# Kernel tuning notes

Hardware: AMD Instinct MI355X
Metric: run time of the kernel (lower is better)

## Reference

```python
import jax, jax.numpy as jnp
import numpy as np

EPS = 1e-5
NUM_HEADS = 8


def _ln(x, w, b):
    m = x.mean(-1, keepdims=True)
    v = jnp.mean(jnp.square(x - m), -1, keepdims=True)
    return (x - m) * jax.lax.rsqrt(v + EPS) * w + b


def _bn(x, w, b, mean, var):  # x: [N, C, T], eval-mode BatchNorm1d
    return (x - mean[None, :, None]) * jax.lax.rsqrt(var[None, :, None] + EPS) * w[None, :, None] + b[None, :, None]


def setup_inputs() -> dict:
    key = jax.random.key(0)
    ks = jax.random.split(key, 32)
    B, T, E, C = 8, 64, 128, 256
    H = 2 * C       # temporal conv hidden
    M = 4 * C       # mlp hidden
    s = 0.02
    f32 = jnp.float32
    inp = {
        'x': jax.random.normal(ks[0], (B, T, E, C), f32),
        'adj_mask': jax.random.randint(ks[1], (E, E), 0, 2, jnp.int32),
        'n1_w': 1.0 + s * jax.random.normal(ks[2], (C,), f32),
        'n1_b': s * jax.random.normal(ks[3], (C,), f32),
        'q_w': s * jax.random.normal(ks[4], (C, C), f32),
        'k_w': s * jax.random.normal(ks[5], (C, C), f32),
        'v_w': s * jax.random.normal(ks[6], (C, C), f32),
        'proj_w': s * jax.random.normal(ks[7], (C, C), f32),
        'proj_b': s * jax.random.normal(ks[8], (C,), f32),
        'on_w': 1.0 + s * jax.random.normal(ks[9], (C,), f32),
        'on_b': s * jax.random.normal(ks[10], (C,), f32),
        'gamma_s': jnp.asarray([0.5], f32),
        'conv1_w': s * jax.random.normal(ks[11], (H, C, 3), f32),
        'bn1_w': 1.0 + s * jax.random.normal(ks[12], (H,), f32),
        'bn1_b': s * jax.random.normal(ks[13], (H,), f32),
        'bn1_m': s * jax.random.normal(ks[14], (H,), f32),
        'bn1_v': jax.random.uniform(ks[15], (H,), f32, 0.5, 1.5),
        'conv2_w': s * jax.random.normal(ks[16], (C, H, 1), f32),
        'bn2_w': 1.0 + s * jax.random.normal(ks[17], (C,), f32),
        'bn2_b': s * jax.random.normal(ks[18], (C,), f32),
        'bn2_m': s * jax.random.normal(ks[19], (C,), f32),
        'bn2_v': jax.random.uniform(ks[20], (C,), f32, 0.5, 1.5),
        'tn_w': 1.0 + s * jax.random.normal(ks[21], (C,), f32),
        'tn_b': s * jax.random.normal(ks[22], (C,), f32),
        'gamma_t': jnp.asarray([0.5], f32),
        'n3_w': 1.0 + s * jax.random.normal(ks[23], (C,), f32),
        'n3_b': s * jax.random.normal(ks[24], (C,), f32),
        'fc1_w': s * jax.random.normal(ks[25], (C, M), f32),
        'fc1_b': s * jax.random.normal(ks[26], (M,), f32),
        'fc2_w': s * jax.random.normal(ks[27], (M, C), f32),
        'fc2_b': s * jax.random.normal(ks[28], (C,), f32),
    }
    return inp


def reference(x, adj_mask, n1_w, n1_b, q_w, k_w, v_w, proj_w, proj_b, on_w, on_b,
              gamma_s, conv1_w, bn1_w, bn1_b, bn1_m, bn1_v, conv2_w, bn2_w, bn2_b,
              bn2_m, bn2_v, tn_w, tn_b, gamma_t, n3_w, n3_b, fc1_w, fc1_b, fc2_w, fc2_b):
    B, T, E, C = x.shape
    Hh = NUM_HEADS
    D = C // Hh
    mask = adj_mask.astype(x.dtype)

    # ---- spatial geometric-cosine attention (per frame) ----
    xs = _ln(x, n1_w, n1_b)                                   # norm1
    q = (xs @ q_w).reshape(B, T, E, Hh, D)
    k = (xs @ k_w).reshape(B, T, E, Hh, D)
    v = (xs @ v_w).reshape(B, T, E, Hh, D)
    attn = jnp.einsum('btehd,btfhd->bthef', q, k)             # [B,T,H,E,E]
    attn = (attn * mask[None, None, None] + 1.0) * 0.5        # affine mask, no softmax
    o = jnp.einsum('bthef,btfhd->btehd', attn, v).reshape(B, T, E, C)
    o = _ln(o @ proj_w + proj_b, on_w, on_b)                  # proj + output_norm
    x = x + (xs + gamma_s * o)                                # inner + outer residual

    # ---- temporal convolution (norm2 is Identity) ----
    xt = _ln(x, tn_w, tn_b)
    xc = xt.transpose(0, 2, 3, 1).reshape(B * E, C, T)        # 'b t e c -> (b e) c t'
    dn = ('NCH', 'OIH', 'NCH')
    y = jax.lax.conv_general_dilated(xc, conv1_w, (1,), [(1, 1)], dimension_numbers=dn)
    y = jax.nn.gelu(_bn(y, bn1_w, bn1_b, bn1_m, bn1_v), approximate=False)
    y = jax.lax.conv_general_dilated(y, conv2_w, (1,), [(0, 0)], dimension_numbers=dn)
    y = _bn(y, bn2_w, bn2_b, bn2_m, bn2_v)
    y = y.reshape(B, E, C, T).transpose(0, 3, 1, 2)           # '(b e) c t -> b t e c'
    x = x + (x + gamma_t * y)                                 # temporal inner + outer residual

    # ---- MLP ----
    xm = _ln(x, n3_w, n3_b)
    h = jax.nn.gelu(xm @ fc1_w + fc1_b, approximate=False)
    x = x + (h @ fc2_w + fc2_b)
    return x
```

## Files before the change

kernel.cpp:

```cpp
#include <hip/hip_runtime.h>
#include <cstdint>

constexpr int Bn = 8, Tn = 64, En = 128, Cn = 256;
constexpr int Hn = 512, Mn = 1024, NHd = 8, Dn = 32;
constexpr int NTOK = Bn * Tn * En;
constexpr size_t SZ = (size_t)NTOK * Cn;
#define EPSF 1e-5f

typedef __attribute__((ext_vector_type(8))) short short8;
typedef __attribute__((ext_vector_type(4))) float f32x4;

__device__ __forceinline__ float bf2f(unsigned short u) {
  union { unsigned int i; float f; } c; c.i = ((unsigned int)u) << 16; return c.f;
}
__device__ __forceinline__ unsigned short f2bf(float f) {
  union { float f; unsigned int i; } c; c.f = f;
  unsigned int u = c.i;
  return (unsigned short)((u + 0x7fffu + ((u >> 16) & 1u)) >> 16);
}
__device__ __forceinline__ float gelu_f(float v) {
  return 0.5f * v * (1.0f + erff(v * 0.70710678118654752440f));
}

__device__ __forceinline__ void gload16(const unsigned short* g, unsigned short* l) {
  __builtin_amdgcn_global_load_lds(
      (const __attribute__((address_space(1))) unsigned int*)g,
      (__attribute__((address_space(3))) unsigned int*)l, 16, 0, 0);
}

template <int EPI, bool C1A>
__global__ __launch_bounds__(256) void mfma_gemm(
    const unsigned short* __restrict__ A,
    const unsigned short* __restrict__ Bt,
    const float* __restrict__ scale,
    const float* __restrict__ bias,
    const float* __restrict__ resf,
    const float* __restrict__ gscal,
    void* __restrict__ outv,
    int K, int N) {
  __shared__ unsigned short As[128 * 32];
  __shared__ unsigned short Bs[128 * 32];
  int tid = threadIdx.x;
  int lane = tid & 63, wave = tid >> 6;
  int mtile = blockIdx.y, ntile = blockIdx.x;
  int rowBase = mtile * 128;
  int colBase = ntile * 128;
  int lda = C1A ? 256 : K;
  int r0 = lane >> 2;
  int c0 = (lane & 3) * 8;
  f32x4 acc[4][4];
#pragma unroll
  for (int i = 0; i < 4; ++i)
#pragma unroll
    for (int j = 0; j < 4; ++j) acc[i][j] = (f32x4)(0.0f);
  int mbase = (wave >> 1) * 64;
  int nbase = (wave & 1) * 64;
  int arow = lane & 15;
  int akk = (lane >> 4) * 8;

  for (int k0 = 0; k0 < K; k0 += 32) {
    size_t arowb; int kin;
    if (C1A) {
      int bb = mtile >> 6, tt = mtile & 63;
      int slab = k0 >> 8;
      arowb = (size_t)((bb * 66 + tt + slab) * 128);
      kin = k0 & 255;
    } else {
      arowb = (size_t)rowBase;
      kin = k0;
    }
#pragma unroll
    for (int i = 0; i < 2; ++i) {
      int q = i * 4 + wave;
      const unsigned short* gp = A + (arowb + q * 16 + r0) * (size_t)lda + kin + c0;
      gload16(gp, &As[q * 512]);
      const unsigned short* gq = Bt + ((size_t)colBase + q * 16 + r0) * (size_t)K + k0 + c0;
      gload16(gq, &Bs[q * 512]);
    }
    __syncthreads();
    short8 af[4], bf[4];
#pragma unroll
    for (int i = 0; i < 4; ++i)
      af[i] = *(const short8*)&As[(mbase + i * 16 + arow) * 32 + akk];
#pragma unroll
    for (int j = 0; j < 4; ++j)
      bf[j] = *(const short8*)&Bs[(nbase + j * 16 + arow) * 32 + akk];
#pragma unroll
    for (int i = 0; i < 4; ++i)
#pragma unroll
      for (int j = 0; j < 4; ++j)
        acc[i][j] = __builtin_amdgcn_mfma_f32_16x16x32_bf16(af[i], bf[j], acc[i][j], 0, 0, 0);
    __syncthreads();
  }

  int crow0 = (lane >> 4) * 4;
  int ccol = lane & 15;
  float gt = (EPI == 3) ? gscal[0] : 0.f;
#pragma unroll
  for (int i = 0; i < 4; ++i) {
#pragma unroll
    for (int j = 0; j < 4; ++j) {
      int col = colBase + nbase + j * 16 + ccol;
      float sc = 1.f, bi = 0.f;
      if (EPI >= 1 && bias) bi = bias[col];
      if ((EPI == 2 || EPI == 3) && scale) sc = scale[col];
#pragma unroll
      for (int r = 0; r < 4; ++r) {
        size_t row = (size_t)rowBase + mbase + i * 16 + crow0 + r;
        size_t idx = row * (size_t)N + col;
        float v = acc[i][j][r];
        if (EPI == 0)      ((unsigned short*)outv)[idx] = f2bf(v);
        else if (EPI == 1) ((unsigned short*)outv)[idx] = f2bf(v + bi);
        else if (EPI == 2) ((unsigned short*)outv)[idx] = f2bf(gelu_f(v * sc + bi));
        else if (EPI == 3) ((float*)outv)[idx] = 2.0f * resf[idx] + gt * (v * sc + bi);
        else if (EPI == 4) ((float*)outv)[idx] = resf[idx] + v + bi;
        else if (EPI == 5) ((float*)outv)[idx] = v + bi;
      }
    }
  }
}

template <bool PAD>
__global__ __launch_bounds__(256) void ln256_bf(const float* __restrict__ src,
                                                const float* __restrict__ w,
                                                const float* __restrict__ b,
                                                unsigned short* __restrict__ dst) {
  int lane = threadIdx.x & 63;
  int tok = blockIdx.x * 4 + (threadIdx.x >> 6);
  const float4* row = (const float4*)(src + (size_t)tok * Cn);
  float4 v = row[lane];
  float s  = v.x + v.y + v.z + v.w;
  float s2 = v.x*v.x + v.y*v.y + v.z*v.z + v.w*v.w;
#pragma unroll
  for (int off = 32; off >= 1; off >>= 1) {
    s  += __shfl_xor(s, off, 64);
    s2 += __shfl_xor(s2, off, 64);
  }
  float mean = s * (1.0f / Cn);
  float var = fmaxf(s2 * (1.0f / Cn) - mean * mean, 0.0f);
  float r = rsqrtf(var + EPSF);
  float4 wv = ((const float4*)w)[lane];
  float4 bv = ((const float4*)b)[lane];
  size_t dtok = tok;
  if (PAD) {
    int bb = tok >> 13, tt = (tok >> 7) & 63, e = tok & 127;
    dtok = ((size_t)(bb * 66 + tt + 1)) * 128 + e;
  }
  ushort4 o;
  o.x = f2bf((v.x - mean) * r * wv.x + bv.x);
  o.y = f2bf((v.y - mean) * r * wv.y + bv.y);
  o.z = f2bf((v.z - mean) * r * wv.z + bv.z);
  o.w = f2bf((v.w - mean) * r * wv.w + bv.w);
  *(ushort4*)(dst + dtok * Cn + lane * 4) = o;
}

__global__ __launch_bounds__(256) void attn_mfma(const unsigned short* __restrict__ qkv,
                                                 const float* __restrict__ maskh,
                                                 unsigned short* __restrict__ o) {
  __shared__ unsigned short Qs[128 * 32];
  __shared__ unsigned short Ks[128 * 32];
  __shared__ unsigned short Vt[32 * 136];
  __shared__ unsigned short Ps[128 * 136];
  int tid = threadIdx.x, lane = tid & 63, wave = tid >> 6;
  int h = blockIdx.x & 7, bt = blockIdx.x >> 3;
  size_t gbase = (size_t)bt * 128 * 768 + h * 32;
#pragma unroll
  for (int i = 0; i < 2; ++i) {
    int q = wave * 2 + i;
    int row = q * 16 + (lane >> 2);
    int seg = (lane & 3) * 8;
    gload16(qkv + gbase + (size_t)row * 768 + seg, &Qs[q * 512]);
    gload16(qkv + gbase + 256 + (size_t)row * 768 + seg, &Ks[q * 512]);
  }
  {
    int e = tid >> 1, dh = (tid & 1) * 16;
    const unsigned short* gv = qkv + gbase + 512 + (size_t)e * 768 + dh;
    short8 v0 = *(const short8*)gv;
    short8 v1 = *(const short8*)(gv + 8);
#pragma unroll
    for (int j = 0; j < 8; ++j) {
      Vt[(dh + j) * 136 + e]     = (unsigned short)v0[j];
      Vt[(dh + 8 + j) * 136 + e] = (unsigned short)v1[j];
    }
  }
  __syncthreads();
  int arow = lane & 15, akk = (lane >> 4) * 8;
  int crow0 = (lane >> 4) * 4, ccol = lane & 15;
  short8 af0 = *(const short8*)&Qs[(wave * 32 + arow) * 32 + akk];
  short8 af1 = *(const short8*)&Qs[(wave * 32 + 16 + arow) * 32 + akk];
#pragma unroll
  for (int j = 0; j < 8; ++j) {
    short8 bfr = *(const short8*)&Ks[(j * 16 + arow) * 32 + akk];
    f32x4 s0 = __builtin_amdgcn_mfma_f32_16x16x32_bf16(af0, bfr, (f32x4)(0.0f), 0, 0, 0);
    f32x4 s1 = __builtin_amdgcn_mfma_f32_16x16x32_bf16(af1, bfr, (f32x4)(0.0f), 0, 0, 0);
    int f = j * 16 + ccol;
#pragma unroll
    for (int r = 0; r < 4; ++r) {
      int e0 = wave * 32 + crow0 + r;
      int e1 = e0 + 16;
      Ps[e0 * 136 + f] = f2bf(maskh[e0 * 128 + f] * s0[r] + 0.5f);
      Ps[e1 * 136 + f] = f2bf(maskh[e1 * 128 + f] * s1[r] + 0.5f);
    }
  }
  f32x4 acc[2][2];
#pragma unroll
  for (int i = 0; i < 2; ++i)
#pragma unroll
    for (int j = 0; j < 2; ++j) acc[i][j] = (f32x4)(0.0f);
#pragma unroll
  for (int k0 = 0; k0 < 128; k0 += 32) {
    short8 a0 = *(const short8*)&Ps[(wave * 32 + arow) * 136 + k0 + akk];
    short8 a1 = *(const short8*)&Ps[(wave * 32 + 16 + arow) * 136 + k0 + akk];
    short8 b0 = *(const short8*)&Vt[arow * 136 + k0 + akk];
    short8 b1 = *(const short8*)&Vt[(16 + arow) * 136 + k0 + akk];
    acc[0][0] = __builtin_amdgcn_mfma_f32_16x16x32_bf16(a0, b0, acc[0][0], 0, 0, 0);
    acc[0][1] = __builtin_amdgcn_mfma_f32_16x16x32_bf16(a0, b1, acc[0][1], 0, 0, 0);
    acc[1][0] = __builtin_amdgcn_mfma_f32_16x16x32_bf16(a1, b0, acc[1][0], 0, 0, 0);
    acc[1][1] = __builtin_amdgcn_mfma_f32_16x16x32_bf16(a1, b1, acc[1][1], 0, 0, 0);
  }
  unsigned short* ob = o + (size_t)bt * 128 * 256 + h * 32;
#pragma unroll
  for (int i = 0; i < 2; ++i)
#pragma unroll
    for (int j = 0; j < 2; ++j)
#pragma unroll
      for (int r = 0; r < 4; ++r) {
        int e = wave * 32 + i * 16 + crow0 + r;
        ob[(size_t)e * 256 + j * 16 + ccol] = f2bf(acc[i][j][r]);
      }
}

__global__ __launch_bounds__(256) void resid1_kernel(const float* __restrict__ x,
                                                     const unsigned short* __restrict__ xs,
                                                     const unsigned short* __restrict__ p2,
                                                     const float* __restrict__ gs,
                                                     float* __restrict__ x1) {
  size_t i = ((size_t)blockIdx.x * 256 + threadIdx.x) * 4;
  float g = gs[0];
  float4 xv = *(const float4*)(x + i);
  ushort4 s4 = *(const ushort4*)(xs + i);
  ushort4 p4 = *(const ushort4*)(p2 + i);
  float4 r;
  r.x = xv.x + bf2f(s4.x) + g * bf2f(p4.x);
  r.y = xv.y + bf2f(s4.y) + g * bf2f(p4.y);
  r.z = xv.z + bf2f(s4.z) + g * bf2f(p4.z);
  r.w = xv.w + bf2f(s4.w) + g * bf2f(p4.w);
  *(float4*)(x1 + i) = r;
}

__global__ __launch_bounds__(256) void transcast(const float* __restrict__ src,
                                                 unsigned short* __restrict__ dst,
                                                 int N, int K) {
  int idx = blockIdx.x * 256 + threadIdx.x;
  int n = idx / K, k = idx - n * K;
  dst[idx] = f2bf(src[(size_t)k * N + n]);
}
__global__ __launch_bounds__(256) void castbf(const float* __restrict__ s,
                                              unsigned short* __restrict__ d) {
  int i = blockIdx.x * 256 + threadIdx.x;
  d[i] = f2bf(s[i]);
}
__global__ __launch_bounds__(256) void pack_conv1(const float* __restrict__ w1,
                                                  unsigned short* __restrict__ dst) {
  int idx = blockIdx.x * 256 + threadIdx.x;
  int hh = idx / 768, kk = idx - hh * 768;
  int slab = kk >> 8, c = kk & 255;
  dst[idx] = f2bf(w1[(size_t)hh * 768 + c * 3 + slab]);
}
__global__ __launch_bounds__(256) void bnfold(const float* __restrict__ w,
                                              const float* __restrict__ bvec,
                                              const float* __restrict__ m,
                                              const float* __restrict__ v,
                                              float* __restrict__ s,
                                              float* __restrict__ o, int n) {
  int i = blockIdx.x * 256 + threadIdx.x;
  if (i < n) {
    float sc = w[i] * rsqrtf(v[i] + EPSF);
    s[i] = sc;
    o[i] = bvec[i] - m[i] * sc;
  }
}
__global__ __launch_bounds__(256) void mask_prep(const int* __restrict__ adj,
                                                 float* __restrict__ maskh) {
  int i = blockIdx.x * 256 + threadIdx.x;
  maskh[i] = 0.5f * (float)adj[i];
}
__global__ __launch_bounds__(256) void zero_pad(unsigned short* __restrict__ xt) {
  int idx = blockIdx.x * 256 + threadIdx.x;
  int bb = idx >> 16;
  int rem = idx & 65535;
  int which = rem >> 15;
  int off = rem & 32767;
  size_t base = ((size_t)(bb * 66 + which * 65)) * 128 * 256;
  xt[base + off] = 0;
}

extern "C" void kernel_launch(void* const* d_in, const int* in_sizes, int n_in,
                              void* d_out, int out_size, void* d_ws, size_t ws_size,
                              hipStream_t stream) {
  (void)in_sizes; (void)n_in; (void)out_size; (void)ws_size;
  const float* x       = (const float*)d_in[0];
  const int*   adj     = (const int*)  d_in[1];
  const float* n1_w    = (const float*)d_in[2];
  const float* n1_b    = (const float*)d_in[3];
  const float* q_w     = (const float*)d_in[4];
  const float* k_w     = (const float*)d_in[5];
  const float* v_w     = (const float*)d_in[6];
  const float* proj_w  = (const float*)d_in[7];
  const float* proj_b  = (const float*)d_in[8];
  const float* on_w    = (const float*)d_in[9];
  const float* on_b    = (const float*)d_in[10];
  const float* gamma_s = (const float*)d_in[11];
  const float* conv1_w = (const float*)d_in[12];
  const float* bn1_w   = (const float*)d_in[13];
  const float* bn1_b   = (const float*)d_in[14];
  const float* bn1_m   = (const float*)d_in[15];
  const float* bn1_v   = (const float*)d_in[16];
  const float* conv2_w = (const float*)d_in[17];
  const float* bn2_w   = (const float*)d_in[18];
  const float* bn2_b   = (const float*)d_in[19];
  const float* bn2_m   = (const float*)d_in[20];
  const float* bn2_v   = (const float*)d_in[21];
  const float* tn_w    = (const float*)d_in[22];
  const float* tn_b    = (const float*)d_in[23];
  const float* gamma_t = (const float*)d_in[24];
  const float* n3_w    = (const float*)d_in[25];
  const float* n3_b    = (const float*)d_in[26];
  const float* fc1_w   = (const float*)d_in[27];
  const float* fc1_b   = (const float*)d_in[28];
  const float* fc2_w   = (const float*)d_in[29];
  const float* fc2_b   = (const float*)d_in[30];
  float* O = (float*)d_out;

  const size_t MB = 1024 * 1024;
  char* wsb = (char*)d_ws;
  unsigned short* qkvb = (unsigned short*)(wsb + 0);
  float*          pjo  = (float*)(wsb + 0);
  float*          x1b  = (float*)(wsb + 0);
  unsigned short* xmb  = (unsigned short*)(wsb + 0);
  unsigned short* hb   = (unsigned short*)(wsb + 32 * MB);
  unsigned short* xtp  = (unsigned short*)(wsb + 64 * MB);
  unsigned short* xsb  = (unsigned short*)(wsb + 96 * MB);
  unsigned short* oat  = (unsigned short*)(wsb + 128 * MB);
  unsigned short* p2b  = (unsigned short*)(wsb + 128 * MB);
  unsigned short* y1b  = (unsigned short*)(wsb + 100 * MB);
  char* wp = wsb + 164 * MB;
  unsigned short* Wqkv = (unsigned short*)wp;  wp += 768 * 256 * 2;
  unsigned short* PjT  = (unsigned short*)wp;  wp += 256 * 256 * 2;
  unsigned short* W1t  = (unsigned short*)wp;  wp += 512 * 768 * 2;
  unsigned short* W2t  = (unsigned short*)wp;  wp += 256 * 512 * 2;
  unsigned short* F1t  = (unsigned short*)wp;  wp += 1024 * 256 * 2;
  unsigned short* F2t  = (unsigned short*)wp;  wp += 256 * 1024 * 2;
  float* s1 = (float*)wp; wp += 512 * 4;
  float* o1 = (float*)wp; wp += 512 * 4;
  float* s2 = (float*)wp; wp += 256 * 4;
  float* o2 = (float*)wp; wp += 256 * 4;
  float* maskh = (float*)wp; wp += 16384 * 4;

  transcast<<<768 * 256 / 256, 256, 0, stream>>>(q_w, Wqkv, 256, 256);
  transcast<<<768 * 256 / 256, 256, 0, stream>>>(k_w, Wqkv + 256 * 256, 256, 256);
  transcast<<<768 * 256 / 256, 256, 0, stream>>>(v_w, Wqkv + 512 * 256, 256, 256);
  transcast<<<256 * 256 / 256, 256, 0, stream>>>(proj_w, PjT, 256, 256);
  pack_conv1<<<512 * 768 / 256, 256, 0, stream>>>(conv1_w, W1t);
  castbf<<<256 * 512 / 256, 256, 0, stream>>>(conv2_w, W2t);
  transcast<<<1024 * 256 / 256, 256, 0, stream>>>(fc1_w, F1t, 1024, 256);
  transcast<<<256 * 1024 / 256, 256, 0, stream>>>(fc2_w, F2t, 256, 1024);
  bnfold<<<2, 256, 0, stream>>>(bn1_w, bn1_b, bn1_m, bn1_v, s1, o1, 512);
  bnfold<<<1, 256, 0, stream>>>(bn2_w, bn2_b, bn2_m, bn2_v, s2, o2, 256);
  mask_prep<<<64, 256, 0, stream>>>(adj, maskh);
  zero_pad<<<524288 / 256, 256, 0, stream>>>(xtp);

  ln256_bf<false><<<NTOK / 4, 256, 0, stream>>>(x, n1_w, n1_b, xsb);
  mfma_gemm<0, false><<<dim3(6, 512), 256, 0, stream>>>(xsb, Wqkv, nullptr, nullptr, nullptr, nullptr, qkvb, 256, 768);
  attn_mfma<<<Bn * Tn * NHd, 256, 0, stream>>>(qkvb, maskh, oat);
  mfma_gemm<5, false><<<dim3(2, 512), 256, 0, stream>>>(oat, PjT, nullptr, proj_b, nullptr, nullptr, pjo, 256, 256);
  ln256_bf<false><<<NTOK / 4, 256, 0, stream>>>(pjo, on_w, on_b, p2b);
  resid1_kernel<<<(int)(SZ / (4 * 256)), 256, 0, stream>>>(x, xsb, p2b, gamma_s, x1b);

  ln256_bf<true><<<NTOK / 4, 256, 0, stream>>>(x1b, tn_w, tn_b, xtp);
  mfma_gemm<2, true><<<dim3(4, 512), 256, 0, stream>>>(xtp, W1t, s1, o1, nullptr, nullptr, y1b, 768, 512);
  mfma_gemm<3, false><<<dim3(2, 512), 256, 0, stream>>>(y1b, W2t, s2, o2, x1b, gamma_t, O, 512, 256);

  ln256_bf<false><<<NTOK / 4, 256, 0, stream>>>(O, n3_w, n3_b, xmb);
  mfma_gemm<2, false><<<dim3(8, 512), 256, 0, stream>>>(xmb, F1t, nullptr, fc1_b, nullptr, nullptr, hb, 256, 1024);
  mfma_gemm<4, false><<<dim3(2, 512), 256, 0, stream>>>(hb, F2t, nullptr, fc2_b, O, nullptr, O, 1024, 256);
}
```

Before: 742.3 us.

## Double-buffer LDS tiles in MFMA GEMM and swizzle workgroups across XCDs

The GEMM main loop now uses two LDS buffers so the global-to-LDS loads for the next K-slice are issued before the MFMAs on the current slice run, with explicit vmcnt waits and barriers replacing the two __syncthreads per iteration. Block indices are also remapped so that consecutive tiles land on the same XCD chiplet, which should improve L2 reuse. The cost is doubled LDS use, which may lower occupancy. The swizzle assumes the grid size is divisible by 8, and the loop assumes an even number of K-steps of at least two.

```diff
diff --git a/kernel.cpp b/kernel.cpp
--- a/kernel.cpp
+++ b/kernel.cpp
@@ -27,6 +27,8 @@
       (const __attribute__((address_space(1))) unsigned int*)g,
       (__attribute__((address_space(3))) unsigned int*)l, 16, 0, 0);
 }
+
+#define MEMFENCE() asm volatile("" ::: "memory")
 
 template <int EPI, bool C1A>
 __global__ __launch_bounds__(256) void mfma_gemm(
@@ -38,11 +40,18 @@
     const float* __restrict__ gscal,
     void* __restrict__ outv,
     int K, int N) {
-  __shared__ unsigned short As[128 * 32];
-  __shared__ unsigned short Bs[128 * 32];
+  __shared__ unsigned short As[2][128 * 32];
+  __shared__ unsigned short Bs[2][128 * 32];
   int tid = threadIdx.x;
   int lane = tid & 63, wave = tid >> 6;
-  int mtile = blockIdx.y, ntile = blockIdx.x;
+
+  int nwg = gridDim.x * gridDim.y;
+  int flat = blockIdx.y * gridDim.x + blockIdx.x;
+  int cpx = nwg >> 3;
+  int swz = (flat & 7) * cpx + (flat >> 3);
+  int ntile = swz % gridDim.x;
+  int mtile = swz / gridDim.x;
+
   int rowBase = mtile * 128;
   int colBase = ntile * 128;
   int lda = C1A ? 256 : K;
@@ -58,7 +67,7 @@
   int arow = lane & 15;
   int akk = (lane >> 4) * 8;
 
-  for (int k0 = 0; k0 < K; k0 += 32) {
+  auto stage = [&](int p, int k0) {
     size_t arowb; int kin;
     if (C1A) {
       int bb = mtile >> 6, tt = mtile & 63;
@@ -72,26 +81,69 @@
 #pragma unroll
     for (int i = 0; i < 2; ++i) {
       int q = i * 4 + wave;
-      const unsigned short* gp = A + (arowb + q * 16 + r0) * (size_t)lda + kin + c0;
-      gload16(gp, &As[q * 512]);
-      const unsigned short* gq = Bt + ((size_t)colBase + q * 16 + r0) * (size_t)K + k0 + c0;
-      gload16(gq, &Bs[q * 512]);
+      gload16(A + (arowb + q * 16 + r0) * (size_t)lda + kin + c0, &As[p][q * 512]);
+      gload16(Bt + ((size_t)colBase + q * 16 + r0) * (size_t)K + k0 + c0, &Bs[p][q * 512]);
     }
-    __syncthreads();
-    short8 af[4], bf[4];
+  };
+  auto compute = [&](int p) {
+    short8 af[4], bfr[4];
 #pragma unroll
     for (int i = 0; i < 4; ++i)
-      af[i] = *(const short8*)&As[(mbase + i * 16 + arow) * 32 + akk];
+      af[i] = *(const short8*)&As[p][(mbase + i * 16 + arow) * 32 + akk];
 #pragma unroll
     for (int j = 0; j < 4; ++j)
-      bf[j] = *(const short8*)&Bs[(nbase + j * 16 + arow) * 32 + akk];
+      bfr[j] = *(const short8*)&Bs[p][(nbase + j * 16 + arow) * 32 + akk];
 #pragma unroll
     for (int i = 0; i < 4; ++i)
 #pragma unroll
       for (int j = 0; j < 4; ++j)
-        acc[i][j] = __builtin_amdgcn_mfma_f32_16x16x32_bf16(af[i], bf[j], acc[i][j], 0, 0, 0);
-    __syncthreads();
-  }
+        acc[i][j] = __builtin_amdgcn_mfma_f32_16x16x32_bf16(af[i], bfr[j], acc[i][j], 0, 0, 0);
+  };
+
+  stage(0, 0);
+  int nk = K >> 5;
+  int t = 0;
+  for (; t < nk - 2; t += 2) {
+    MEMFENCE();
+    __builtin_amdgcn_s_barrier();
+    MEMFENCE();
+    stage(1, (t + 1) << 5);
+    asm volatile("s_waitcnt vmcnt(4)" ::: "memory");
+    __builtin_amdgcn_sched_barrier(0);
+    __builtin_amdgcn_s_barrier();
+    MEMFENCE();
+    __builtin_amdgcn_sched_barrier(0);
+    compute(0);
+    MEMFENCE();
+    __builtin_amdgcn_s_barrier();
+    MEMFENCE();
+    stage(0, (t + 2) << 5);
+    asm volatile("s_waitcnt vmcnt(4)" ::: "memory");
+    __builtin_amdgcn_sched_barrier(0);
+    __builtin_amdgcn_s_barrier();
+    MEMFENCE();
+    __builtin_amdgcn_sched_barrier(0);
+    compute(1);
+  }
+  MEMFENCE();
+  __builtin_amdgcn_s_barrier();
+  MEMFENCE();
+  stage(1, (t + 1) << 5);
+  asm volatile("s_waitcnt vmcnt(4)" ::: "memory");
+  __builtin_amdgcn_sched_barrier(0);
+  __builtin_amdgcn_s_barrier();
+  MEMFENCE();
+  __builtin_amdgcn_sched_barrier(0);
+  compute(0);
+  MEMFENCE();
+  __builtin_amdgcn_s_barrier();
+  asm volatile("s_waitcnt vmcnt(0)" ::: "memory");
+  __builtin_amdgcn_sched_barrier(0);
+  __builtin_amdgcn_s_barrier();
+  MEMFENCE();
+  __builtin_amdgcn_sched_barrier(0);
+  compute(1);
+  MEMFENCE();
 
   int crow0 = (lane >> 4) * 4;
   int ccol = lane & 15;
```

After: 693.9 us. 1.07x faster.

## Rewrite GEMM as 256x256 tiles with 4-stage async LDS pipeline and fast GELU

Applied to the files above, without the earlier changes.

The GEMM kernel moves to 512-thread blocks computing 256x256 output tiles. It uses a four-slot LDS ring filled by asynchronous global-to-LDS loads issued three k-steps ahead, with explicit vmcnt waits and MFMA priority hints. An XCD-aware block swizzle is added to improve cache locality. GELU's erf is replaced by a sigmoid-based approximation built on exp2 and rcp, which cuts epilogue cost but changes numerics slightly. The larger tiles raise register and LDS pressure and may lower occupancy.

```diff
diff --git a/kernel.cpp b/kernel.cpp
--- a/kernel.cpp
+++ b/kernel.cpp
@@ -19,7 +19,10 @@
   return (unsigned short)((u + 0x7fffu + ((u >> 16) & 1u)) >> 16);
 }
 __device__ __forceinline__ float gelu_f(float v) {
-  return 0.5f * v * (1.0f + erff(v * 0.70710678118654752440f));
+  float x2 = v * v;
+  float p = v * fmaf(x2, 0.10294532f, 2.30221000f);
+  float d = 1.0f + __builtin_amdgcn_exp2f(-p);
+  return v * __builtin_amdgcn_rcpf(d);
 }
 
 __device__ __forceinline__ void gload16(const unsigned short* g, unsigned short* l) {
@@ -28,8 +31,10 @@
       (__attribute__((address_space(3))) unsigned int*)l, 16, 0, 0);
 }
 
+#define MEMFENCE() asm volatile("" ::: "memory")
+
 template <int EPI, bool C1A>
-__global__ __launch_bounds__(256) void mfma_gemm(
+__global__ __launch_bounds__(512) void mfma_gemm(
     const unsigned short* __restrict__ A,
     const unsigned short* __restrict__ Bt,
     const float* __restrict__ scale,
@@ -38,83 +43,133 @@
     const float* __restrict__ gscal,
     void* __restrict__ outv,
     int K, int N) {
-  __shared__ unsigned short As[128 * 32];
-  __shared__ unsigned short Bs[128 * 32];
+  __shared__ unsigned short lds[4][2][8192];
   int tid = threadIdx.x;
   int lane = tid & 63, wave = tid >> 6;
-  int mtile = blockIdx.y, ntile = blockIdx.x;
-  int rowBase = mtile * 128;
-  int colBase = ntile * 128;
+  int wr = wave >> 2, wc = wave & 3;
+
+  int nwg = gridDim.x * gridDim.y;
+  int flat = blockIdx.y * gridDim.x + blockIdx.x;
+  int cpx = nwg >> 3;
+  int swz = (flat & 7) * cpx + (flat >> 3);
+  int ntile = swz % gridDim.x;
+  int mtile = swz / gridDim.x;
+  int rowBase = mtile * 256;
+  int colBase = ntile * 256;
   int lda = C1A ? 256 : K;
-  int r0 = lane >> 2;
-  int c0 = (lane & 3) * 8;
-  f32x4 acc[4][4];
-#pragma unroll
-  for (int i = 0; i < 4; ++i)
-#pragma unroll
-    for (int j = 0; j < 4; ++j) acc[i][j] = (f32x4)(0.0f);
-  int mbase = (wave >> 1) * 64;
-  int nbase = (wave & 1) * 64;
-  int arow = lane & 15;
-  int akk = (lane >> 4) * 8;
-
-  for (int k0 = 0; k0 < K; k0 += 32) {
-    size_t arowb; int kin;
-    if (C1A) {
-      int bb = mtile >> 6, tt = mtile & 63;
-      int slab = k0 >> 8;
-      arowb = (size_t)((bb * 66 + tt + slab) * 128);
-      kin = k0 & 255;
-    } else {
-      arowb = (size_t)rowBase;
-      kin = k0;
+
+  int arow = lane & 15, g8 = (lane >> 4) * 8;
+  int aoff[8], boff[4];
+#pragma unroll
+  for (int m = 0; m < 8; ++m) aoff[m] = (wr * 128 + m * 16 + arow) * 32 + g8;
+#pragma unroll
+  for (int n = 0; n < 4; ++n) boff[n] = (wc * 64 + n * 16 + arow) * 32 + g8;
+
+  f32x4 acc[8][4];
+#pragma unroll
+  for (int m = 0; m < 8; ++m)
+#pragma unroll
+    for (int n = 0; n < 4; ++n) acc[m][n] = (f32x4)(0.0f);
+
+  int srow = lane >> 2;
+  int scol = (lane & 3) * 8;
+
+  auto stageA = [&](int T) {
+    int k0 = T << 5, slot = T & 3;
+#pragma unroll
+    for (int r = 0; r < 2; ++r) {
+      int row = r * 128 + wave * 16 + srow;
+      const unsigned short* src;
+      if (C1A) {
+        int idx = rowBase + row;
+        int bb = idx >> 13, tt = (idx >> 7) & 63, e = idx & 127;
+        src = A + ((size_t)((bb * 66 + tt + (k0 >> 8)) * 128 + e)) * 256 +
+              (k0 & 255) + scol;
+      } else {
+        src = A + (size_t)(rowBase + row) * lda + k0 + scol;
+      }
+      gload16(src, &lds[slot][0][r * 4096 + wave * 512]);
     }
-#pragma unroll
-    for (int i = 0; i < 2; ++i) {
-      int q = i * 4 + wave;
-      const unsigned short* gp = A + (arowb + q * 16 + r0) * (size_t)lda + kin + c0;
-      gload16(gp, &As[q * 512]);
-      const unsigned short* gq = Bt + ((size_t)colBase + q * 16 + r0) * (size_t)K + k0 + c0;
-      gload16(gq, &Bs[q * 512]);
+  };
+  auto stageB = [&](int T) {
+    int k0 = T << 5, slot = T & 3;
+#pragma unroll
+    for (int r = 0; r < 2; ++r) {
+      int row = r * 128 + wave * 16 + srow;
+      const unsigned short* src = Bt + (size_t)(colBase + row) * K + k0 + scol;
+      gload16(src, &lds[slot][1][r * 4096 + wave * 512]);
     }
-    __syncthreads();
-    short8 af[4], bf[4];
-#pragma unroll
-    for (int i = 0; i < 4; ++i)
-      af[i] = *(const short8*)&As[(mbase + i * 16 + arow) * 32 + akk];
-#pragma unroll
-    for (int j = 0; j < 4; ++j)
-      bf[j] = *(const short8*)&Bs[(nbase + j * 16 + arow) * 32 + akk];
-#pragma unroll
-    for (int i = 0; i < 4; ++i)
-#pragma unroll
-      for (int j = 0; j < 4; ++j)
-        acc[i][j] = __builtin_amdgcn_mfma_f32_16x16x32_bf16(af[i], bf[j], acc[i][j], 0, 0, 0);
-    __syncthreads();
-  }
-
-  int crow0 = (lane >> 4) * 4;
-  int ccol = lane & 15;
+  };
+
+  auto tile = [&](int T, int vm, bool st) {
+    if (vm == 8)      asm volatile("s_waitcnt vmcnt(8)" ::: "memory");
+    else if (vm == 4) asm volatile("s_waitcnt vmcnt(4)" ::: "memory");
+    else              asm volatile("s_waitcnt vmcnt(0)" ::: "memory");
+    __builtin_amdgcn_sched_barrier(0);
+    __builtin_amdgcn_s_barrier();
+    MEMFENCE();
+    if (st) stageA(T + 3);
+    const unsigned short* as = &lds[T & 3][0][0];
+    const unsigned short* bs = &lds[T & 3][1][0];
+    short8 bfr[4], af[4];
+#pragma unroll
+    for (int n = 0; n < 4; ++n) bfr[n] = *(const short8*)(bs + boff[n]);
+#pragma unroll
+    for (int m = 0; m < 4; ++m) af[m] = *(const short8*)(as + aoff[m]);
+    __builtin_amdgcn_s_setprio(1);
+#pragma unroll
+    for (int m = 0; m < 4; ++m)
+#pragma unroll
+      for (int n = 0; n < 4; ++n)
+        acc[m][n] = __builtin_amdgcn_mfma_f32_16x16x32_bf16(af[m], bfr[n], acc[m][n], 0, 0, 0);
+    __builtin_amdgcn_s_setprio(0);
+    if (st) stageB(T + 3);
+#pragma unroll
+    for (int m = 0; m < 4; ++m) af[m] = *(const short8*)(as + aoff[4 + m]);
+    __builtin_amdgcn_s_setprio(1);
+#pragma unroll
+    for (int m = 0; m < 4; ++m)
+#pragma unroll
+      for (int n = 0; n < 4; ++n)
+        acc[4 + m][n] = __builtin_amdgcn_mfma_f32_16x16x32_bf16(af[m], bfr[n], acc[4 + m][n], 0, 0, 0);
+    __builtin_amdgcn_s_setprio(0);
+  };
+
+  stageA(0); stageB(0); stageA(1); stageB(1); stageA(2); stageB(2);
+  int nkt = K >> 5;
+  for (int T = 0; T < nkt - 3; ++T) tile(T, 8, true);
+  tile(nkt - 3, 8, false);
+  tile(nkt - 2, 4, false);
+  tile(nkt - 1, 0, false);
+  MEMFENCE();
+
+  int crow0 = (lane >> 4) * 4, ccol = lane & 15;
+  size_t rb = (size_t)rowBase + wr * 128;
+  int cb = colBase + wc * 64;
   float gt = (EPI == 3) ? gscal[0] : 0.f;
-#pragma unroll
-  for (int i = 0; i < 4; ++i) {
-#pragma unroll
-    for (int j = 0; j < 4; ++j) {
-      int col = colBase + nbase + j * 16 + ccol;
-      float sc = 1.f, bi = 0.f;
-      if (EPI >= 1 && bias) bi = bias[col];
-      if ((EPI == 2 || EPI == 3) && scale) sc = scale[col];
+  float bi[4], sc[4];
+#pragma unroll
+  for (int n = 0; n < 4; ++n) {
+    int col = cb + n * 16 + ccol;
+    bi[n] = (EPI >= 1 && bias) ? bias[col] : 0.f;
+    sc[n] = ((EPI == 2 || EPI == 3) && scale) ? scale[col] : 1.f;
+  }
+#pragma unroll
+  for (int m = 0; m < 8; ++m) {
+#pragma unroll
+    for (int n = 0; n < 4; ++n) {
+      int col = cb + n * 16 + ccol;
 #pragma unroll
       for (int r = 0; r < 4; ++r) {
-        size_t row = (size_t)rowBase + mbase + i * 16 + crow0 + r;
+        size_t row = rb + m * 16 + crow0 + r;
         size_t idx = row * (size_t)N + col;
-        float v = acc[i][j][r];
+        float v = acc[m][n][r];
         if (EPI == 0)      ((unsigned short*)outv)[idx] = f2bf(v);
-        else if (EPI == 1) ((unsigned short*)outv)[idx] = f2bf(v + bi);
-        else if (EPI == 2) ((unsigned short*)outv)[idx] = f2bf(gelu_f(v * sc + bi));
-        else if (EPI == 3) ((float*)outv)[idx] = 2.0f * resf[idx] + gt * (v * sc + bi);
-        else if (EPI == 4) ((float*)outv)[idx] = resf[idx] + v + bi;
-        else if (EPI == 5) ((float*)outv)[idx] = v + bi;
+        else if (EPI == 1) ((unsigned short*)outv)[idx] = f2bf(v + bi[n]);
+        else if (EPI == 2) ((unsigned short*)outv)[idx] = f2bf(gelu_f(v * sc[n] + bi[n]));
+        else if (EPI == 3) ((float*)outv)[idx] = 2.0f * resf[idx] + gt * (v * sc[n] + bi[n]);
+        else if (EPI == 4) ((float*)outv)[idx] = resf[idx] + v + bi[n];
+        else if (EPI == 5) ((float*)outv)[idx] = v + bi[n];
       }
     }
   }
@@ -371,17 +426,17 @@
   zero_pad<<<524288 / 256, 256, 0, stream>>>(xtp);
 
   ln256_bf<false><<<NTOK / 4, 256, 0, stream>>>(x, n1_w, n1_b, xsb);
-  mfma_gemm<0, false><<<dim3(6, 512), 256, 0, stream>>>(xsb, Wqkv, nullptr, nullptr, nullptr, nullptr, qkvb, 256, 768);
+  mfma_gemm<0, false><<<dim3(3, 256), 512, 0, stream>>>(xsb, Wqkv, nullptr, nullptr, nullptr, nullptr, qkvb, 256, 768);
   attn_mfma<<<Bn * Tn * NHd, 256, 0, stream>>>(qkvb, maskh, oat);
-  mfma_gemm<5, false><<<dim3(2, 512), 256, 0, stream>>>(oat, PjT, nullptr, proj_b, nullptr, nullptr, pjo, 256, 256);
+  mfma_gemm<5, false><<<dim3(1, 256), 512, 0, stream>>>(oat, PjT, nullptr, proj_b, nullptr, nullptr, pjo, 256, 256);
   ln256_bf<false><<<NTOK / 4, 256, 0, stream>>>(pjo, on_w, on_b, p2b);
   resid1_kernel<<<(int)(SZ / (4 * 256)), 256, 0, stream>>>(x, xsb, p2b, gamma_s, x1b);
 
   ln256_bf<true><<<NTOK / 4, 256, 0, stream>>>(x1b, tn_w, tn_b, xtp);
-  mfma_gemm<2, true><<<dim3(4, 512), 256, 0, stream>>>(xtp, W1t, s1, o1, nullptr, nullptr, y1b, 768, 512);
-  mfma_gemm<3, false><<<dim3(2, 512), 256, 0, stream>>>(y1b, W2t, s2, o2, x1b, gamma_t, O, 512, 256);
+  mfma_gemm<2, true><<<dim3(2, 256), 512, 0, stream>>>(xtp, W1t, s1, o1, nullptr, nullptr, y1b, 768, 512);
+  mfma_gemm<3, false><<<dim3(1, 256), 512, 0, stream>>>(y1b, W2t, s2, o2, x1b, gamma_t, O, 512, 256);
 
   ln256_bf<false><<<NTOK / 4, 256, 0, stream>>>(O, n3_w, n3_b, xmb);
-  mfma_gemm<2, false><<<dim3(8, 512), 256, 0, stream>>>(xmb, F1t, nullptr, fc1_b, nullptr, nullptr, hb, 256, 1024);
-  mfma_gemm<4, false><<<dim3(2, 512), 256, 0, stream>>>(hb, F2t, nullptr, fc2_b, O, nullptr, O, 1024, 256);
-}
+  mfma_gemm<2, false><<<dim3(4, 256), 512, 0, stream>>>(xmb, F1t, nullptr, fc1_b, nullptr, nullptr, hb, 256, 1024);
+  mfma_gemm<4, false><<<dim3(1, 256), 512, 0, stream>>>(hb, F2t, nullptr, fc2_b, O, nullptr, O, 1024, 256);
+}
```

Measured after the change: 607.5 us. 1.22x faster.
